# Kernel optimization log

Measured on AMD Instinct MI355X. Metric: run time of the kernel, lower is better.

Reference implementation:

```python
import jax, jax.numpy as jnp
import numpy as np

B, S, D = 1, 2048, 2048
HQ, HKV, HD = 32, 4, 128
E, K, F = 8, 2, 768
EPS = 1e-6
ROPE_THETA = 1000000.0


def rmsnorm(x, scale, eps=EPS):
    var = jnp.mean(jnp.square(x), axis=-1, keepdims=True)
    return x * jax.lax.rsqrt(var + eps) * scale


def rotate_half(x):
    h = x.shape[-1] // 2
    return jnp.concatenate([-x[..., h:], x[..., :h]], axis=-1)


def rope_cos_sin(seq_len, head_dim, dtype=jnp.float32):
    inv_freq = 1.0 / (ROPE_THETA ** (jnp.arange(0, head_dim, 2, dtype=jnp.float32) / head_dim))
    angles = jnp.arange(seq_len, dtype=jnp.float32)[:, None] * inv_freq[None, :]  # (S, HD/2)
    emb = jnp.concatenate([angles, angles], axis=-1)  # (S, HD)
    return jnp.cos(emb).astype(dtype), jnp.sin(emb).astype(dtype)


def setup_inputs() -> dict:
    key = jax.random.key(0)
    ks = jax.random.split(key, 16)
    s = lambda i, shape, scale: jax.random.normal(ks[i], shape, dtype=jnp.float32) * scale
    inp = {
        "hidden_states": s(0, (B, S, D), 1.0),
        "ln1_scale": jnp.ones((D,), jnp.float32),
        "ln2_scale": jnp.ones((D,), jnp.float32),
        "Wq": s(1, (D, HQ * HD), 0.02),
        "Wk": s(2, (D, HKV * HD), 0.02),
        "Wv": s(3, (D, HKV * HD), 0.02),
        "Wo": s(4, (HQ * HD, D), 0.02),
        "q_norm_scale": jnp.ones((HD,), jnp.float32),
        "k_norm_scale": jnp.ones((HD,), jnp.float32),
        "router_W": s(5, (D, E), 0.02),
        "up_W": s(6, (E, D, F), 0.02),
        "up_b": jnp.zeros((E, F), jnp.float32),
        "down_W": s(7, (E, F, D), 0.02),
        "down_b": jnp.zeros((E, D), jnp.float32),
    }
    return inp


def reference(hidden_states, ln1_scale, ln2_scale, Wq, Wk, Wv, Wo,
              q_norm_scale, k_norm_scale, router_W, up_W, up_b, down_W, down_b):
    b, s_len, d = hidden_states.shape
    # ---- pre-norm + self-attention ----
    residual = hidden_states
    x = rmsnorm(hidden_states, ln1_scale)
    q = (x @ Wq).reshape(b, s_len, HQ, HD)
    k = (x @ Wk).reshape(b, s_len, HKV, HD)
    v = (x @ Wv).reshape(b, s_len, HKV, HD)
    q = rmsnorm(q, q_norm_scale)
    k = rmsnorm(k, k_norm_scale)
    cos, sin = rope_cos_sin(s_len, HD, q.dtype)
    cos = cos[None, :, None, :]
    sin = sin[None, :, None, :]
    q = q * cos + rotate_half(q) * sin
    k = k * cos + rotate_half(k) * sin
    g = HQ // HKV
    k = jnp.repeat(k, g, axis=2)  # (b, s, HQ, HD)
    v = jnp.repeat(v, g, axis=2)
    scores = jnp.einsum('bqhd,bkhd->bhqk', q, k) / jnp.sqrt(jnp.asarray(HD, q.dtype))
    causal = jnp.tril(jnp.ones((s_len, s_len), bool))
    scores = jnp.where(causal[None, None], scores, jnp.asarray(-1e9, scores.dtype))
    probs = jax.nn.softmax(scores, axis=-1)
    attn = jnp.einsum('bhqk,bkhd->bqhd', probs, v).reshape(b, s_len, HQ * HD)
    attn_out = attn @ Wo
    hidden = residual + attn_out
    # ---- pre-norm + dense-all-experts MoE ----
    residual = hidden
    xf = rmsnorm(hidden, ln2_scale).reshape(-1, d)  # (T, D)
    router_logits = xf @ router_W  # (T, E)
    routing_weights = jax.nn.softmax(router_logits, axis=-1)
    gating_weights, selected = jax.lax.top_k(routing_weights, K)  # (T, K)
    gating_weights = gating_weights / jnp.sum(gating_weights, axis=-1, keepdims=True)
    expert_mask = jax.nn.one_hot(selected, E, dtype=gating_weights.dtype)  # (T, K, E)
    h = jax.nn.silu(jnp.einsum('td,edf->tef', xf, up_W) + up_b[None])  # (T, E, F)
    expert_outputs = jnp.einsum('tef,efd->ted', h, down_W) + down_b[None]  # (T, E, D)
    weighted = jnp.einsum('tke,ted->tkd', expert_mask, expert_outputs)  # (T, K, D)
    moe_out = jnp.sum(weighted * gating_weights[..., None], axis=1).reshape(b, s_len, d)
    hidden = residual + moe_out
    # ---- load balancing auxiliary loss (no attention mask path) ----
    expert_usage = jnp.mean(jnp.mean(expert_mask, axis=0), axis=0) * E  # (E,)
    su = jnp.sum(expert_usage)
    aux_loss = su * su / (E * E)
    return hidden, router_logits, aux_loss
```

## Files before the change

kernel.cpp:

```cpp
#include <hip/hip_runtime.h>
#include <cmath>

typedef __bf16 bf16_t;
typedef __bf16 bf16x8 __attribute__((ext_vector_type(8)));
typedef __bf16 bf16x4 __attribute__((ext_vector_type(4)));
typedef float  f32x4  __attribute__((ext_vector_type(4)));

#define SLEN 2048
#define DMOD 2048
#define NHQ  32
#define NHKV 4
#define HD   128
#define NQC  4096
#define NKVC 512
#define NQKVC 5120
#define NEXP 8
#define NF   768

#define KSTR 136
#define VSTR 72
#define PSTR 72

__device__ __forceinline__ float wredsum(float v) {
#pragma unroll
  for (int off = 32; off > 0; off >>= 1) v += __shfl_xor(v, off);
  return v;
}

__device__ __forceinline__ void gll16(const bf16_t* g, bf16_t* l) {
  __builtin_amdgcn_global_load_lds((const __attribute__((address_space(1))) void*)g,
                                   (__attribute__((address_space(3))) void*)l, 16, 0, 0);
}

__global__ void rope_table_k(float* __restrict__ cosT, float* __restrict__ sinT) {
  int idx = blockIdx.x * 256 + threadIdx.x;
  if (idx >= SLEN * 64) return;
  int t = idx >> 6, j = idx & 63;
  double inv = exp(-0.2158673524681918 * (double)j);
  double ang = (double)t * inv;
  cosT[idx] = (float)cos(ang);
  sinT[idx] = (float)sin(ang);
}

__global__ __launch_bounds__(256) void transpose_split2_k(const float* __restrict__ in,
                                                          bf16_t* __restrict__ outH,
                                                          bf16_t* __restrict__ outL,
                                                          int R, int C) {
  __shared__ float tile[32][33];
  int tx = threadIdx.x, ty = threadIdx.y;
  int c0 = blockIdx.x * 32, r0 = blockIdx.y * 32;
#pragma unroll
  for (int i = 0; i < 4; i++)
    tile[ty + i * 8][tx] = in[(size_t)(r0 + ty + i * 8) * C + c0 + tx];
  __syncthreads();
#pragma unroll
  for (int i = 0; i < 4; i++) {
    int c = c0 + ty + i * 8;
    int r = r0 + tx;
    float w = tile[tx][ty + i * 8];
    bf16_t hi = (bf16_t)w;
    bf16_t lo = (bf16_t)(w - (float)hi);
    size_t o = (size_t)c * R + r;
    outH[o] = hi;
    outL[o] = lo;
  }
}

__global__ __launch_bounds__(256) void transpose_plain_k(const float* __restrict__ in,
                                                         bf16_t* __restrict__ out,
                                                         int R, int C) {
  __shared__ float tile[32][33];
  int b = blockIdx.z;
  const float* inb = in + (size_t)b * R * C;
  bf16_t* outb = out + (size_t)b * R * C;
  int tx = threadIdx.x, ty = threadIdx.y;
  int c0 = blockIdx.x * 32, r0 = blockIdx.y * 32;
#pragma unroll
  for (int i = 0; i < 4; i++)
    tile[ty + i * 8][tx] = inb[(size_t)(r0 + ty + i * 8) * C + c0 + tx];
  __syncthreads();
#pragma unroll
  for (int i = 0; i < 4; i++) {
    int c = c0 + ty + i * 8;
    int r = r0 + tx;
    outb[(size_t)c * R + r] = (bf16_t)tile[tx][ty + i * 8];
  }
}

__global__ __launch_bounds__(256) void rmsnorm1_k(const float* __restrict__ hs,
                                                  const float* __restrict__ sc,
                                                  bf16_t* __restrict__ xnH,
                                                  bf16_t* __restrict__ xnL) {
  const int t = blockIdx.x;
  const float* row = hs + (size_t)t * DMOD;
  const int tid = threadIdx.x;
  const int i0 = tid * 8;
  float4 a = *(const float4*)(row + i0);
  float4 b = *(const float4*)(row + i0 + 4);
  float x[8] = {a.x, a.y, a.z, a.w, b.x, b.y, b.z, b.w};
  float ss = 0.f;
#pragma unroll
  for (int j = 0; j < 8; j++) ss += x[j] * x[j];
  ss = wredsum(ss);
  __shared__ float red[4];
  if ((tid & 63) == 0) red[tid >> 6] = ss;
  __syncthreads();
  float rn = rsqrtf((red[0] + red[1] + red[2] + red[3]) * (1.f / 2048.f) + 1e-6f);
#pragma unroll
  for (int j = 0; j < 8; j++) {
    float v = x[j] * rn * sc[i0 + j];
    bf16_t hi = (bf16_t)v;
    bf16_t lo = (bf16_t)(v - (float)hi);
    xnH[(size_t)t * DMOD + i0 + j] = hi;
    xnL[(size_t)t * DMOD + i0 + j] = lo;
  }
}

template <bool RESID>
__global__ __launch_bounds__(256) void gemm_split128_k(const bf16_t* __restrict__ Ah,
                                                       const bf16_t* __restrict__ Al,
                                                       int lda,
                                                       const bf16_t* __restrict__ Bh,
                                                       const bf16_t* __restrict__ Bl,
                                                       int ldb, int K,
                                                       const float* __restrict__ resid,
                                                       float* __restrict__ C, int ldc) {
  __shared__ bf16_t AsH[128][32], AsL[128][32], BsH[128][32], BsL[128][32];
  const int t = threadIdx.x;
  const int w = t >> 6, lane = t & 63;
  const int m16 = lane & 15, quad = lane >> 4;
  const int m0 = blockIdx.y * 128, n0 = blockIdx.x * 128;
  const int wm = (w & 1) * 64, wn = (w >> 1) * 64;
  f32x4 acc[4][4];
#pragma unroll
  for (int i = 0; i < 4; i++)
#pragma unroll
    for (int j = 0; j < 4; j++) acc[i][j] = (f32x4){0.f, 0.f, 0.f, 0.f};

  const int srow = t >> 2;
  const int scol = (t & 3) * 8;
  const int lw = w * 512;
  const bf16_t* gAh0 = Ah + (size_t)(m0 + srow) * lda + scol;
  const bf16_t* gAh1 = Ah + (size_t)(m0 + 64 + srow) * lda + scol;
  const bf16_t* gAl0 = Al + (size_t)(m0 + srow) * lda + scol;
  const bf16_t* gAl1 = Al + (size_t)(m0 + 64 + srow) * lda + scol;
  const bf16_t* gBh0 = Bh + (size_t)(n0 + srow) * ldb + scol;
  const bf16_t* gBh1 = Bh + (size_t)(n0 + 64 + srow) * ldb + scol;
  const bf16_t* gBl0 = Bl + (size_t)(n0 + srow) * ldb + scol;
  const bf16_t* gBl1 = Bl + (size_t)(n0 + 64 + srow) * ldb + scol;

  for (int k0 = 0; k0 < K; k0 += 32) {
    __syncthreads();
    gll16(gAh0 + k0, &AsH[0][0] + lw);
    gll16(gAh1 + k0, &AsH[0][0] + 2048 + lw);
    gll16(gAl0 + k0, &AsL[0][0] + lw);
    gll16(gAl1 + k0, &AsL[0][0] + 2048 + lw);
    gll16(gBh0 + k0, &BsH[0][0] + lw);
    gll16(gBh1 + k0, &BsH[0][0] + 2048 + lw);
    gll16(gBl0 + k0, &BsL[0][0] + lw);
    gll16(gBl1 + k0, &BsL[0][0] + 2048 + lw);
    __syncthreads();
    bf16x8 a_h[4], a_l[4];
#pragma unroll
    for (int mt = 0; mt < 4; mt++) {
      a_h[mt] = *(const bf16x8*)(&AsH[wm + mt * 16 + m16][quad * 8]);
      a_l[mt] = *(const bf16x8*)(&AsL[wm + mt * 16 + m16][quad * 8]);
    }
#pragma unroll
    for (int nt = 0; nt < 4; nt++) {
      bf16x8 b_h = *(const bf16x8*)(&BsH[wn + nt * 16 + m16][quad * 8]);
      bf16x8 b_l = *(const bf16x8*)(&BsL[wn + nt * 16 + m16][quad * 8]);
#pragma unroll
      for (int mt = 0; mt < 4; mt++) {
        acc[mt][nt] = __builtin_amdgcn_mfma_f32_16x16x32_bf16(a_h[mt], b_h, acc[mt][nt], 0, 0, 0);
        acc[mt][nt] = __builtin_amdgcn_mfma_f32_16x16x32_bf16(a_l[mt], b_h, acc[mt][nt], 0, 0, 0);
        acc[mt][nt] = __builtin_amdgcn_mfma_f32_16x16x32_bf16(a_h[mt], b_l, acc[mt][nt], 0, 0, 0);
      }
    }
  }
#pragma unroll
  for (int mt = 0; mt < 4; mt++)
#pragma unroll
    for (int r = 0; r < 4; r++) {
      const size_t row = m0 + wm + mt * 16 + quad * 4 + r;
#pragma unroll
      for (int nt = 0; nt < 4; nt++) {
        const size_t idx = row * ldc + n0 + wn + nt * 16 + m16;
        if (RESID) C[idx] = acc[mt][nt][r] + resid[idx];
        else       C[idx] = acc[mt][nt][r];
      }
    }
}

template <class AROW>
__device__ __forceinline__ void gemm_core(AROW getA, const bf16_t* __restrict__ Bt, int ldb,
                                          int n0, int K, f32x4 acc[4]) {
  __shared__ bf16_t As[64][32];
  __shared__ bf16_t Bs[64][32];
  const int t = threadIdx.x;
  const int wave = t >> 6, lane = t & 63;
  const int m16 = lane & 15, quad = lane >> 4;
  const int sr = t >> 2, sc = (t & 3) << 3;
  const bf16_t* __restrict__ arow = getA(sr);
  const bf16_t* __restrict__ brow = Bt + (size_t)(n0 + sr) * ldb;
  for (int k0 = 0; k0 < K; k0 += 32) {
    __syncthreads();
    *(uint4*)(&As[sr][sc]) = *(const uint4*)(arow + k0 + sc);
    *(uint4*)(&Bs[sr][sc]) = *(const uint4*)(brow + k0 + sc);
    __syncthreads();
    bf16x8 af = *(const bf16x8*)(&As[wave * 16 + m16][quad * 8]);
#pragma unroll
    for (int nt = 0; nt < 4; nt++) {
      bf16x8 bfr = *(const bf16x8*)(&Bs[nt * 16 + m16][quad * 8]);
      acc[nt] = __builtin_amdgcn_mfma_f32_16x16x32_bf16(af, bfr, acc[nt], 0, 0, 0);
    }
  }
}

__global__ __launch_bounds__(128) void qknorm_rope_k(float* __restrict__ qkv,
                                                     const float* __restrict__ qsc,
                                                     const float* __restrict__ ksc,
                                                     const float* __restrict__ cosT,
                                                     const float* __restrict__ sinT) {
  const int t = blockIdx.x;
  const int hh = blockIdx.y;
  const bool isq = hh < NHQ;
  float* ptr = qkv + (size_t)t * NQKVC + (isq ? hh * HD : NQC + (hh - NHQ) * HD);
  const int i = threadIdx.x;
  float x = ptr[i];
  float ss = x * x;
  ss = wredsum(ss);
  __shared__ float red2[2];
  __shared__ float xs[128];
  if ((i & 63) == 0) red2[i >> 6] = ss;
  __syncthreads();
  float rn = rsqrtf((red2[0] + red2[1]) * (1.f / 128.f) + 1e-6f);
  float xn = x * rn * (isq ? qsc[i] : ksc[i]);
  xs[i] = xn;
  __syncthreads();
  int j = i & 63;
  float c = cosT[t * 64 + j];
  float s = sinT[t * 64 + j];
  float rot = (i < 64) ? -xs[i + 64] : xs[i - 64];
  ptr[i] = xn * c + rot * s;
}

__global__ __launch_bounds__(256) void kprep_k(const float* __restrict__ qkv,
                                               bf16_t* __restrict__ Kh,
                                               bf16_t* __restrict__ Kl) {
  const int gid = blockIdx.x * 256 + threadIdx.x;
  const int tok = gid >> 6;
  const int c = (gid & 63) * 8;
  const int hk = c >> 7, d = c & 127;
  const float* p = qkv + (size_t)tok * NQKVC + NQC + c;
  float4 a = *(const float4*)p;
  float4 b = *(const float4*)(p + 4);
  float xv[8] = {a.x, a.y, a.z, a.w, b.x, b.y, b.z, b.w};
  bf16x8 hv, lv;
#pragma unroll
  for (int j = 0; j < 8; j++) {
    bf16_t hi = (bf16_t)xv[j];
    hv[j] = hi;
    lv[j] = (bf16_t)(xv[j] - (float)hi);
  }
  const size_t o = ((size_t)hk * SLEN + tok) * HD + d;
  *(bf16x8*)(Kh + o) = hv;
  *(bf16x8*)(Kl + o) = lv;
}

__global__ __launch_bounds__(256) void vprep_k(const float* __restrict__ qkv,
                                               bf16_t* __restrict__ Vh,
                                               bf16_t* __restrict__ Vl) {
  __shared__ float tile[32][33];
  const int hk = blockIdx.z;
  const int tx = threadIdx.x, ty = threadIdx.y;
  const int t0 = blockIdx.x * 32, d0 = blockIdx.y * 32;
#pragma unroll
  for (int i = 0; i < 4; i++)
    tile[ty + i * 8][tx] =
        qkv[(size_t)(t0 + ty + i * 8) * NQKVC + NQC + NKVC + hk * HD + d0 + tx];
  __syncthreads();
#pragma unroll
  for (int i = 0; i < 4; i++) {
    int d = d0 + ty + i * 8;
    int tk = t0 + tx;
    float wv = tile[tx][ty + i * 8];
    bf16_t hi = (bf16_t)wv;
    size_t o = ((size_t)hk * HD + d) * SLEN + tk;
    Vh[o] = hi;
    Vl[o] = (bf16_t)(wv - (float)hi);
  }
}

__global__ __launch_bounds__(256) void attn_mfma_k(const float* __restrict__ qkv,
                                                   const bf16_t* __restrict__ Kph,
                                                   const bf16_t* __restrict__ Kpl,
                                                   const bf16_t* __restrict__ Vph,
                                                   const bf16_t* __restrict__ Vpl,
                                                   bf16_t* __restrict__ attnH,
                                                   bf16_t* __restrict__ attnL) {
  const int bx = blockIdx.x;
  const int hh = blockIdx.y;
  const int hk = hh >> 3;
  __shared__ bf16_t sK[2][64][KSTR];
  __shared__ bf16_t sV[2][128][VSTR];
  const int t = threadIdx.x;
  const int w = t >> 6, lane = t & 63;
  const int m16 = lane & 15, quad = lane >> 4;
  const float SCALE = 0.08838834764831845f;

  const int ksr = t >> 4;
  const int ksc = (t & 15) * 8;
  const int vsd = t >> 3;
  const int vsk = (t & 7) * 8;
  const bf16_t* KbH = Kph + (size_t)hk * SLEN * HD;
  const bf16_t* KbL = Kpl + (size_t)hk * SLEN * HD;
  const bf16_t* VbH = Vph + (size_t)hk * HD * SLEN;
  const bf16_t* VbL = Vpl + (size_t)hk * HD * SLEN;
  bf16_t* sP = &sK[0][0][0];

  for (int half = 0; half < 2; half++) {
    const int qb = half ? bx : 31 - bx;

    bf16x8 Qh[4], Ql[4];
    {
      const int qrow = qb * 64 + w * 16 + m16;
      const float* qp = qkv + (size_t)qrow * NQKVC + hh * HD + quad * 8;
#pragma unroll
      for (int kc = 0; kc < 4; kc++) {
        float4 x0 = *(const float4*)(qp + kc * 32);
        float4 x1 = *(const float4*)(qp + kc * 32 + 4);
        float xv[8] = {x0.x, x0.y, x0.z, x0.w, x1.x, x1.y, x1.z, x1.w};
#pragma unroll
        for (int j = 0; j < 8; j++) {
          bf16_t hi = (bf16_t)xv[j];
          Qh[kc][j] = hi;
          Ql[kc][j] = (bf16_t)(xv[j] - (float)hi);
        }
      }
    }
    f32x4 acc[8];
#pragma unroll
    for (int i = 0; i < 8; i++) acc[i] = (f32x4){0.f, 0.f, 0.f, 0.f};
    float mrow[4], lrow[4];
#pragma unroll
    for (int r = 0; r < 4; r++) { mrow[r] = -1e30f; lrow[r] = 0.f; }

    for (int kb = 0; kb <= qb; kb++) {
      __syncthreads();
      {
#pragma unroll
        for (int i = 0; i < 4; i++) {
          const int row = ksr + i * 16;
          const size_t go = (size_t)(kb * 64 + row) * HD + ksc;
          *(bf16x8*)(&sK[0][row][ksc]) = *(const bf16x8*)(KbH + go);
          *(bf16x8*)(&sK[1][row][ksc]) = *(const bf16x8*)(KbL + go);
        }
      }
      {
#pragma unroll
        for (int i = 0; i < 4; i++) {
          const int d = vsd + i * 32;
          const size_t go = (size_t)d * SLEN + kb * 64 + vsk;
          *(bf16x8*)(&sV[0][d][vsk]) = *(const bf16x8*)(VbH + go);
          *(bf16x8*)(&sV[1][d][vsk]) = *(const bf16x8*)(VbL + go);
        }
      }
      __syncthreads();
      f32x4 xs[4];
#pragma unroll
      for (int nt = 0; nt < 4; nt++) {
        f32x4 s = (f32x4){0.f, 0.f, 0.f, 0.f};
        if (kb < qb || nt <= w) {
#pragma unroll
          for (int kc = 0; kc < 4; kc++) {
            bf16x8 kh = *(const bf16x8*)(&sK[0][nt * 16 + m16][kc * 32 + quad * 8]);
            bf16x8 kl = *(const bf16x8*)(&sK[1][nt * 16 + m16][kc * 32 + quad * 8]);
            s = __builtin_amdgcn_mfma_f32_16x16x32_bf16(Qh[kc], kh, s, 0, 0, 0);
            s = __builtin_amdgcn_mfma_f32_16x16x32_bf16(Ql[kc], kh, s, 0, 0, 0);
            s = __builtin_amdgcn_mfma_f32_16x16x32_bf16(Qh[kc], kl, s, 0, 0, 0);
          }
        }
        xs[nt] = s;
      }
      __syncthreads();
      float p[4][4], alpha[4];
#pragma unroll
      for (int r = 0; r < 4; r++) {
        const int rqg = qb * 64 + w * 16 + quad * 4 + r;
        float xr[4];
#pragma unroll
        for (int nt = 0; nt < 4; nt++) {
          int colg = kb * 64 + nt * 16 + m16;
          xr[nt] = (colg <= rqg) ? xs[nt][r] * SCALE : -1e30f;
        }
        float mx = fmaxf(fmaxf(xr[0], xr[1]), fmaxf(xr[2], xr[3]));
#pragma unroll
        for (int off = 1; off < 16; off <<= 1) mx = fmaxf(mx, __shfl_xor(mx, off));
        float mn = fmaxf(mrow[r], mx);
        float al = __expf(mrow[r] - mn);
        float rs = 0.f;
#pragma unroll
        for (int nt = 0; nt < 4; nt++) {
          float pv = __expf(xr[nt] - mn);
          p[nt][r] = pv;
          rs += pv;
        }
#pragma unroll
        for (int off = 1; off < 16; off <<= 1) rs += __shfl_xor(rs, off);
        lrow[r] = lrow[r] * al + rs;
        mrow[r] = mn;
        alpha[r] = al;
      }
#pragma unroll
      for (int dt = 0; dt < 8; dt++)
#pragma unroll
        for (int r = 0; r < 4; r++) acc[dt][r] *= alpha[r];
      {
        bf16_t* base = sP + (size_t)w * 2 * 16 * PSTR;
#pragma unroll
        for (int nt = 0; nt < 4; nt++)
#pragma unroll
          for (int r = 0; r < 4; r++) {
            float pv = p[nt][r];
            bf16_t hi = (bf16_t)pv;
            base[(quad * 4 + r) * PSTR + nt * 16 + m16] = hi;
            base[16 * PSTR + (quad * 4 + r) * PSTR + nt * 16 + m16] = (bf16_t)(pv - (float)hi);
          }
      }
      {
        const bf16_t* base = sP + (size_t)w * 2 * 16 * PSTR;
        bf16x8 Ph[2], Pl[2];
#pragma unroll
        for (int kc = 0; kc < 2; kc++) {
          Ph[kc] = *(const bf16x8*)(base + m16 * PSTR + kc * 32 + quad * 8);
          Pl[kc] = *(const bf16x8*)(base + 16 * PSTR + m16 * PSTR + kc * 32 + quad * 8);
        }
#pragma unroll
        for (int dt = 0; dt < 8; dt++)
#pragma unroll
          for (int kc = 0; kc < 2; kc++) {
            bf16x8 vh = *(const bf16x8*)(&sV[0][dt * 16 + m16][kc * 32 + quad * 8]);
            bf16x8 vl = *(const bf16x8*)(&sV[1][dt * 16 + m16][kc * 32 + quad * 8]);
            acc[dt] = __builtin_amdgcn_mfma_f32_16x16x32_bf16(Ph[kc], vh, acc[dt], 0, 0, 0);
            acc[dt] = __builtin_amdgcn_mfma_f32_16x16x32_bf16(Pl[kc], vh, acc[dt], 0, 0, 0);
            acc[dt] = __builtin_amdgcn_mfma_f32_16x16x32_bf16(Ph[kc], vl, acc[dt], 0, 0, 0);
          }
      }
    }
#pragma unroll
    for (int r = 0; r < 4; r++) {
      const int tok = qb * 64 + w * 16 + quad * 4 + r;
      const float linv = 1.f / lrow[r];
      const size_t ro = (size_t)tok * NQC + hh * HD;
#pragma unroll
      for (int dt = 0; dt < 8; dt++) {
        float v = acc[dt][r] * linv;
        bf16_t hi = (bf16_t)v;
        attnH[ro + dt * 16 + m16] = hi;
        attnL[ro + dt * 16 + m16] = (bf16_t)(v - (float)hi);
      }
    }
  }
}

__global__ __launch_bounds__(256) void rmsnorm2_router_k(const float* __restrict__ hid,
                                                         const float* __restrict__ sc2,
                                                         const float* __restrict__ rW,
                                                         bf16_t* __restrict__ xf,
                                                         float* __restrict__ rlog) {
  const int t = blockIdx.x;
  const float* row = hid + (size_t)t * DMOD;
  const int tid = threadIdx.x;
  const int i0 = tid * 8;
  float4 a = *(const float4*)(row + i0);
  float4 b = *(const float4*)(row + i0 + 4);
  float x[8] = {a.x, a.y, a.z, a.w, b.x, b.y, b.z, b.w};
  float ss = 0.f;
#pragma unroll
  for (int j = 0; j < 8; j++) ss += x[j] * x[j];
  ss = wredsum(ss);
  __shared__ float red[4];
  if ((tid & 63) == 0) red[tid >> 6] = ss;
  __syncthreads();
  float rn = rsqrtf((red[0] + red[1] + red[2] + red[3]) * (1.f / 2048.f) + 1e-6f);
  float acc[8];
#pragma unroll
  for (int e = 0; e < 8; e++) acc[e] = 0.f;
#pragma unroll
  for (int j = 0; j < 8; j++) {
    float xn = x[j] * rn * sc2[i0 + j];
    xf[(size_t)t * DMOD + i0 + j] = (bf16_t)xn;
    const float* w = rW + (size_t)(i0 + j) * NEXP;
#pragma unroll
    for (int e = 0; e < 8; e++) acc[e] += xn * w[e];
  }
#pragma unroll
  for (int e = 0; e < 8; e++) acc[e] = wredsum(acc[e]);
  __shared__ float wacc[4][8];
  if ((tid & 63) == 0)
#pragma unroll
    for (int e = 0; e < 8; e++) wacc[tid >> 6][e] = acc[e];
  __syncthreads();
  if (tid < 8) rlog[t * NEXP + tid] = wacc[0][tid] + wacc[1][tid] + wacc[2][tid] + wacc[3][tid];
}

__global__ void topk_k(const float* __restrict__ rlog, int* __restrict__ sel,
                       float* __restrict__ gates, float* __restrict__ aux) {
  int t = blockIdx.x * 256 + threadIdx.x;
  if (t == 0) aux[0] = 1.0f;
  if (t >= SLEN) return;
  const float* l = rlog + t * NEXP;
  int i1 = 0; float v1 = l[0];
#pragma unroll
  for (int e = 1; e < 8; e++) if (l[e] > v1) { v1 = l[e]; i1 = e; }
  int i2 = -1; float v2 = -1e30f;
#pragma unroll
  for (int e = 0; e < 8; e++) if (e != i1 && l[e] > v2) { v2 = l[e]; i2 = e; }
  float e21 = expf(v2 - v1);
  float inv = 1.f / (1.f + e21);
  sel[t * 2 + 0] = i1;
  sel[t * 2 + 1] = i2;
  gates[t * 2 + 0] = inv;
  gates[t * 2 + 1] = e21 * inv;
}

__global__ void scatter_k(const int* __restrict__ sel, const float* __restrict__ gates,
                          int* __restrict__ cnt, int* __restrict__ tok,
                          float* __restrict__ gateL) {
  int i = blockIdx.x * 256 + threadIdx.x;
  if (i >= SLEN * 2) return;
  int e = sel[i];
  int pos = atomicAdd(&cnt[e], 1);
  tok[e * SLEN + pos] = i >> 1;
  gateL[e * SLEN + pos] = gates[i];
}

__global__ __launch_bounds__(256) void gemm_up_k(const bf16_t* __restrict__ xf,
                                                 const bf16_t* __restrict__ upWT,
                                                 const int* __restrict__ cnt,
                                                 const int* __restrict__ tok,
                                                 const float* __restrict__ up_b,
                                                 bf16_t* __restrict__ hbuf) {
  const int e = blockIdx.z;
  const int c = cnt[e];
  const int m0 = blockIdx.y * 64;
  if (m0 >= c) return;
  const int n0 = blockIdx.x * 64;
  const int* tokE = tok + e * SLEN;
  const bf16_t* BtE = upWT + (size_t)e * NF * DMOD;
  f32x4 zz = {0.f, 0.f, 0.f, 0.f};
  f32x4 acc[4] = {zz, zz, zz, zz};
  gemm_core([=](int r) {
      int s = m0 + r; if (s >= c) s = c - 1;
      return xf + (size_t)tokE[s] * DMOD;
    }, BtE, DMOD, n0, DMOD, acc);
  const int t = threadIdx.x, wave = t >> 6, lane = t & 63;
  const int m16 = lane & 15, quad = lane >> 4;
  const int mb = m0 + wave * 16 + quad * 4;
  const int nb = n0 + m16;
#pragma unroll
  for (int nt = 0; nt < 4; nt++)
#pragma unroll
    for (int r = 0; r < 4; r++) {
      int slot = mb + r;
      if (slot < c) {
        int n = nb + nt * 16;
        float x = acc[nt][r] + up_b[e * NF + n];
        float v = x / (1.f + __expf(-x));
        hbuf[((size_t)e * SLEN + slot) * NF + n] = (bf16_t)v;
      }
    }
}

__global__ __launch_bounds__(256) void gemm_down_k(const bf16_t* __restrict__ hbuf,
                                                   const bf16_t* __restrict__ downWT,
                                                   const int* __restrict__ cnt,
                                                   const int* __restrict__ tok,
                                                   const float* __restrict__ gateL,
                                                   const float* __restrict__ down_b,
                                                   float* __restrict__ outH) {
  const int e = blockIdx.z;
  const int c = cnt[e];
  const int m0 = blockIdx.y * 64;
  if (m0 >= c) return;
  const int n0 = blockIdx.x * 64;
  const bf16_t* Ah = hbuf + (size_t)e * SLEN * NF;
  const bf16_t* BtE = downWT + (size_t)e * DMOD * NF;
  f32x4 zz = {0.f, 0.f, 0.f, 0.f};
  f32x4 acc[4] = {zz, zz, zz, zz};
  gemm_core([=](int r) { return Ah + (size_t)(m0 + r) * NF; }, BtE, NF, n0, NF, acc);
  const int t = threadIdx.x, wave = t >> 6, lane = t & 63;
  const int m16 = lane & 15, quad = lane >> 4;
  const int mb = m0 + wave * 16 + quad * 4;
  const int nb = n0 + m16;
#pragma unroll
  for (int nt = 0; nt < 4; nt++)
#pragma unroll
    for (int r = 0; r < 4; r++) {
      int slot = mb + r;
      if (slot < c) {
        int n = nb + nt * 16;
        int tk = tok[e * SLEN + slot];
        float g = gateL[e * SLEN + slot];
        atomicAdd(&outH[(size_t)tk * DMOD + n], g * (acc[nt][r] + down_b[e * DMOD + n]));
      }
    }
}

extern "C" void kernel_launch(void* const* d_in, const int* in_sizes, int n_in,
                              void* d_out, int out_size, void* d_ws, size_t ws_size,
                              hipStream_t stream) {
  (void)in_sizes; (void)n_in; (void)out_size;
  const float* hs   = (const float*)d_in[0];
  const float* ln1  = (const float*)d_in[1];
  const float* ln2  = (const float*)d_in[2];
  const float* Wq   = (const float*)d_in[3];
  const float* Wk   = (const float*)d_in[4];
  const float* Wv   = (const float*)d_in[5];
  const float* Wo   = (const float*)d_in[6];
  const float* qns  = (const float*)d_in[7];
  const float* kns  = (const float*)d_in[8];
  const float* rW   = (const float*)d_in[9];
  const float* upW  = (const float*)d_in[10];
  const float* upB  = (const float*)d_in[11];
  const float* dnW  = (const float*)d_in[12];
  const float* dnB  = (const float*)d_in[13];
  float* dout = (float*)d_out;

  const size_t NEED = 135431168ull;
  if (ws_size < NEED) return;
  char* ws = (char*)d_ws;
  const size_t OA = 0;
  const size_t OB = OA + 41943040ull;
  const size_t OC = OB + 33554432ull;
  const size_t OD = OC + 16777216ull;
  const size_t OE = OD + 41943040ull;

  bf16_t* BqkvH  = (bf16_t*)(ws + OA);
  bf16_t* BqkvL  = (bf16_t*)(ws + OA + 20971520ull);
  bf16_t* attnH  = (bf16_t*)(ws + OA);
  bf16_t* attnL  = (bf16_t*)(ws + OA + 16777216ull);
  bf16_t* Kph    = (bf16_t*)(ws + OA + 33554432ull);
  bf16_t* Kpl    = Kph + 1048576;
  bf16_t* Vph    = Kpl + 1048576;
  bf16_t* Vpl    = Vph + 1048576;
  bf16_t* upWT   = (bf16_t*)(ws + OA);
  bf16_t* WoH    = (bf16_t*)(ws + OB);
  bf16_t* WoL    = (bf16_t*)(ws + OB + 16777216ull);
  bf16_t* hbuf   = (bf16_t*)(ws + OB);
  bf16_t* xnH    = (bf16_t*)(ws + OC);
  bf16_t* xnL    = (bf16_t*)(ws + OC + 8388608ull);
  bf16_t* xf     = (bf16_t*)(ws + OC);
  float*  qkv    = (float*)(ws + OD);
  bf16_t* downWT = (bf16_t*)(ws + OD);
  float*  cosT   = (float*)(ws + OE);
  float*  sinT   = (float*)(ws + OE + 524288ull);
  int*    sel    = (int*)(ws + OE + 1048576ull);
  float*  gates  = (float*)(ws + OE + 1064960ull);
  int*    cnt    = (int*)(ws + OE + 1081344ull);
  int*    tok    = (int*)(ws + OE + 1082368ull);
  float*  gateL  = (float*)(ws + OE + 1147904ull);

  hipMemsetAsync(cnt, 0, 1024, stream);
  rope_table_k<<<512, 256, 0, stream>>>(cosT, sinT);

  dim3 tb(32, 8);
  transpose_split2_k<<<dim3(128, 64), tb, 0, stream>>>(Wq, BqkvH, BqkvL, 2048, 4096);
  transpose_split2_k<<<dim3(16, 64), tb, 0, stream>>>(Wk, BqkvH + (size_t)4096 * 2048,
                                                      BqkvL + (size_t)4096 * 2048, 2048, 512);
  transpose_split2_k<<<dim3(16, 64), tb, 0, stream>>>(Wv, BqkvH + (size_t)4608 * 2048,
                                                      BqkvL + (size_t)4608 * 2048, 2048, 512);
  transpose_split2_k<<<dim3(64, 128), tb, 0, stream>>>(Wo, WoH, WoL, 4096, 2048);

  rmsnorm1_k<<<2048, 256, 0, stream>>>(hs, ln1, xnH, xnL);
  gemm_split128_k<false><<<dim3(40, 16), 256, 0, stream>>>(xnH, xnL, 2048, BqkvH, BqkvL,
                                                           2048, 2048, nullptr, qkv, NQKVC);
  qknorm_rope_k<<<dim3(2048, 36), 128, 0, stream>>>(qkv, qns, kns, cosT, sinT);
  kprep_k<<<512, 256, 0, stream>>>(qkv, Kph, Kpl);
  vprep_k<<<dim3(64, 4, 4), tb, 0, stream>>>(qkv, Vph, Vpl);
  attn_mfma_k<<<dim3(16, 32), 256, 0, stream>>>(qkv, Kph, Kpl, Vph, Vpl, attnH, attnL);
  gemm_split128_k<true><<<dim3(16, 16), 256, 0, stream>>>(attnH, attnL, 4096, WoH, WoL,
                                                          4096, 4096, hs, dout, DMOD);

  rmsnorm2_router_k<<<2048, 256, 0, stream>>>(dout, ln2, rW, xf, dout + 4194304);
  topk_k<<<8, 256, 0, stream>>>(dout + 4194304, sel, gates, dout + 4210688);
  scatter_k<<<16, 256, 0, stream>>>(sel, gates, cnt, tok, gateL);

  transpose_plain_k<<<dim3(24, 64, 8), tb, 0, stream>>>(upW, upWT, 2048, 768);
  transpose_plain_k<<<dim3(64, 24, 8), tb, 0, stream>>>(dnW, downWT, 768, 2048);

  gemm_up_k<<<dim3(12, 32, 8), 256, 0, stream>>>(xf, upWT, cnt, tok, upB, hbuf);
  gemm_down_k<<<dim3(32, 32, 8), 256, 0, stream>>>(hbuf, downWT, cnt, tok, gateL, dnB, dout);
}
```

Measured before the change: 926.9 us.

## Double-buffer LDS tiles in split-bf16 GEMM and remap blocks for XCD locality

```diff
diff --git a/kernel.cpp b/kernel.cpp
--- a/kernel.cpp
+++ b/kernel.cpp
@@ -125,11 +125,16 @@
                                                        int ldb, int K,
                                                        const float* __restrict__ resid,
                                                        float* __restrict__ C, int ldc) {
-  __shared__ bf16_t AsH[128][32], AsL[128][32], BsH[128][32], BsL[128][32];
+  __shared__ bf16_t AsH[2][128][32], AsL[2][128][32], BsH[2][128][32], BsL[2][128][32];
   const int t = threadIdx.x;
   const int w = t >> 6, lane = t & 63;
   const int m16 = lane & 15, quad = lane >> 4;
-  const int m0 = blockIdx.y * 128, n0 = blockIdx.x * 128;
+  const int nwg = gridDim.x * gridDim.y;
+  const int flat = blockIdx.y * gridDim.x + blockIdx.x;
+  int tile = flat;
+  if ((nwg & 7) == 0) tile = (flat & 7) * (nwg >> 3) + (flat >> 3);
+  const int bx = tile % gridDim.x, by = tile / gridDim.x;
+  const int m0 = by * 128, n0 = bx * 128;
   const int wm = (w & 1) * 64, wn = (w >> 1) * 64;
   f32x4 acc[4][4];
 #pragma unroll
@@ -149,27 +154,39 @@
   const bf16_t* gBl0 = Bl + (size_t)(n0 + srow) * ldb + scol;
   const bf16_t* gBl1 = Bl + (size_t)(n0 + 64 + srow) * ldb + scol;
 
-  for (int k0 = 0; k0 < K; k0 += 32) {
-    __syncthreads();
-    gll16(gAh0 + k0, &AsH[0][0] + lw);
-    gll16(gAh1 + k0, &AsH[0][0] + 2048 + lw);
-    gll16(gAl0 + k0, &AsL[0][0] + lw);
-    gll16(gAl1 + k0, &AsL[0][0] + 2048 + lw);
-    gll16(gBh0 + k0, &BsH[0][0] + lw);
-    gll16(gBh1 + k0, &BsH[0][0] + 2048 + lw);
-    gll16(gBl0 + k0, &BsL[0][0] + lw);
-    gll16(gBl1 + k0, &BsL[0][0] + 2048 + lw);
-    __syncthreads();
+  auto stage = [&](int buf, int k0) {
+    gll16(gAh0 + k0, &AsH[buf][0][0] + lw);
+    gll16(gAh1 + k0, &AsH[buf][0][0] + 2048 + lw);
+    gll16(gAl0 + k0, &AsL[buf][0][0] + lw);
+    gll16(gAl1 + k0, &AsL[buf][0][0] + 2048 + lw);
+    gll16(gBh0 + k0, &BsH[buf][0][0] + lw);
+    gll16(gBh1 + k0, &BsH[buf][0][0] + 2048 + lw);
+    gll16(gBl0 + k0, &BsL[buf][0][0] + lw);
+    gll16(gBl1 + k0, &BsL[buf][0][0] + 2048 + lw);
+  };
+
+  stage(0, 0);
+  int cur = 0;
+  for (int k0 = 32; k0 <= K; k0 += 32) {
+    if (k0 < K) {
+      stage(cur ^ 1, k0);
+      asm volatile("s_waitcnt vmcnt(8)" ::: "memory");
+    } else {
+      asm volatile("s_waitcnt vmcnt(0)" ::: "memory");
+    }
+    __builtin_amdgcn_sched_barrier(0);
+    __builtin_amdgcn_s_barrier();
+    __builtin_amdgcn_sched_barrier(0);
     bf16x8 a_h[4], a_l[4];
 #pragma unroll
     for (int mt = 0; mt < 4; mt++) {
-      a_h[mt] = *(const bf16x8*)(&AsH[wm + mt * 16 + m16][quad * 8]);
-      a_l[mt] = *(const bf16x8*)(&AsL[wm + mt * 16 + m16][quad * 8]);
+      a_h[mt] = *(const bf16x8*)(&AsH[cur][wm + mt * 16 + m16][quad * 8]);
+      a_l[mt] = *(const bf16x8*)(&AsL[cur][wm + mt * 16 + m16][quad * 8]);
     }
 #pragma unroll
     for (int nt = 0; nt < 4; nt++) {
-      bf16x8 b_h = *(const bf16x8*)(&BsH[wn + nt * 16 + m16][quad * 8]);
-      bf16x8 b_l = *(const bf16x8*)(&BsL[wn + nt * 16 + m16][quad * 8]);
+      bf16x8 b_h = *(const bf16x8*)(&BsH[cur][wn + nt * 16 + m16][quad * 8]);
+      bf16x8 b_l = *(const bf16x8*)(&BsL[cur][wn + nt * 16 + m16][quad * 8]);
 #pragma unroll
       for (int mt = 0; mt < 4; mt++) {
         acc[mt][nt] = __builtin_amdgcn_mfma_f32_16x16x32_bf16(a_h[mt], b_h, acc[mt][nt], 0, 0, 0);
@@ -177,6 +194,10 @@
         acc[mt][nt] = __builtin_amdgcn_mfma_f32_16x16x32_bf16(a_h[mt], b_l, acc[mt][nt], 0, 0, 0);
       }
     }
+    __builtin_amdgcn_sched_barrier(0);
+    __builtin_amdgcn_s_barrier();
+    __builtin_amdgcn_sched_barrier(0);
+    cur ^= 1;
   }
 #pragma unroll
   for (int mt = 0; mt < 4; mt++)
```

New measurement: 926.0 us. No clear change (-0.1%).
